# Kernel tuning notes

Measured on AMD Instinct MI355X. Metric: run time of the kernel, lower is better.

The kernel has to match this reference:

```python
import jax, jax.numpy as jnp
import numpy as np

N = 3000          # num_nodes
B = 1             # batch
T_IN = 12
T_OUT = 12
F_IN = 2
F_OUT = 2
HEADS = 8
HID = 32          # hidden_dim (GAT out channels, LSTM hidden)
E = 32000         # directed edges (before self-loops)
NEG_SLOPE = 0.2   # PyG GATConv leaky_relu slope


def setup_inputs() -> dict:
    key = jax.random.key(0)
    ks = jax.random.split(key, 20)
    s = 0.1
    inp = {
        "X": jax.random.normal(ks[0], (B, N, T_IN, F_IN), jnp.float32),
        "edge_index": jax.random.randint(ks[1], (2, E), 0, N, dtype=jnp.int64),
        # GATConv params (shared lin for src/dst, concat=False -> bias of size HID)
        "gat_w": jax.random.normal(ks[2], (HEADS * HID, F_IN), jnp.float32) * s,
        "att_src": jax.random.normal(ks[3], (HEADS, HID), jnp.float32) * s,
        "att_dst": jax.random.normal(ks[4], (HEADS, HID), jnp.float32) * s,
        "gat_b": jax.random.normal(ks[5], (HID,), jnp.float32) * s,
        # 2-layer LSTM, PyTorch gate order (i, f, g, o)
        "w_ih0": jax.random.normal(ks[6], (4 * HID, HID), jnp.float32) * s,
        "w_hh0": jax.random.normal(ks[7], (4 * HID, HID), jnp.float32) * s,
        "b_ih0": jax.random.normal(ks[8], (4 * HID,), jnp.float32) * s,
        "b_hh0": jax.random.normal(ks[9], (4 * HID,), jnp.float32) * s,
        "w_ih1": jax.random.normal(ks[10], (4 * HID, HID), jnp.float32) * s,
        "w_hh1": jax.random.normal(ks[11], (4 * HID, HID), jnp.float32) * s,
        "b_ih1": jax.random.normal(ks[12], (4 * HID,), jnp.float32) * s,
        "b_hh1": jax.random.normal(ks[13], (4 * HID,), jnp.float32) * s,
        # final head: HID -> F_OUT * T_OUT
        "fc_w": jax.random.normal(ks[14], (F_OUT * T_OUT, HID), jnp.float32) * s,
        "fc_b": jax.random.normal(ks[15], (F_OUT * T_OUT,), jnp.float32) * s,
    }
    return inp


def _lstm_layer(xs, w_ih, w_hh, b_ih, b_hh):
    # xs: (T, BN, D) -> hidden states (T, BN, H)
    Hd = w_hh.shape[1]
    def step(carry, x):
        h, c = carry
        g = x @ w_ih.T + h @ w_hh.T + b_ih + b_hh
        i, f, gg, o = jnp.split(g, 4, axis=-1)
        c = jax.nn.sigmoid(f) * c + jax.nn.sigmoid(i) * jnp.tanh(gg)
        h = jax.nn.sigmoid(o) * jnp.tanh(c)
        return (h, c), h
    z = jnp.zeros((xs.shape[1], Hd), xs.dtype)
    _, hs = jax.lax.scan(step, (z, z), xs)
    return hs


def reference(X, edge_index, gat_w, att_src, att_dst, gat_b,
              w_ih0, w_hh0, b_ih0, b_hh0, w_ih1, w_hh1, b_ih1, b_hh1,
              fc_w, fc_b):
    Bb, Nn, T, F = X.shape
    BN = Bb * Nn
    H, C = att_src.shape

    # (T, BN, F), all timesteps processed at once (GAT params shared across t)
    Xr = X.transpose(2, 0, 1, 3).reshape(T, BN, F)
    h = (Xr @ gat_w.T).reshape(T, BN, H, C)          # shared lin for src/dst
    a_s = (h * att_src).sum(-1)                      # (T, BN, H)
    a_d = (h * att_dst).sum(-1)

    # add self-loops (PyG GATConv default) over all BN nodes
    loops = jnp.arange(BN, dtype=edge_index.dtype)
    src = jnp.concatenate([edge_index[0], loops])
    dst = jnp.concatenate([edge_index[1], loops])

    # edge attention logits, edge axis leading for segment ops: (Etot, T, H)
    e = jax.nn.leaky_relu(a_s[:, src] + a_d[:, dst], NEG_SLOPE)
    e = jnp.moveaxis(e, 1, 0)

    # segment softmax over incoming edges per destination node
    m = jax.ops.segment_max(e, dst, num_segments=BN)
    ex = jnp.exp(e - m[dst])
    den = jax.ops.segment_sum(ex, dst, num_segments=BN)
    alpha = ex / den[dst]                            # (Etot, T, H)

    h_node = jnp.moveaxis(h, 0, 1)                   # (BN, T, H, C)
    msg = alpha[..., None] * h_node[src]             # (Etot, T, H, C)
    agg = jax.ops.segment_sum(msg, dst, num_segments=BN)  # (BN, T, H, C)
    gat_out = agg.mean(2) + gat_b                    # concat=False -> head mean; (BN, T, C)

    # 2-layer LSTM over time
    xs = gat_out.transpose(1, 0, 2)                  # (T, BN, C)
    hs = _lstm_layer(xs, w_ih0, w_hh0, b_ih0, b_hh0)
    hs = _lstm_layer(hs, w_ih1, w_hh1, b_ih1, b_hh1)
    h_last = hs[-1]                                  # (BN, HID)

    out = h_last @ fc_w.T + fc_b                     # (BN, F_OUT*T_OUT)
    return out.reshape(Bb, Nn, T_OUT, F)
```

## Files before the change

### kernel.cpp

```cpp
#include <hip/hip_runtime.h>
#include <math.h>

#define N_NODES 3000
#define T_STEPS 12
#define F_INP 2
#define HEADS 8
#define HID 32
#define E_EDGES 32000
#define E_TOT (E_EDGES + N_NODES)
#define NEG_SLOPE 0.2f
#define OUT_F 24
#define SLOTS 48
#define CHUNKS 6
#define NT (N_NODES * T_STEPS)
#define WROW 33

__device__ __forceinline__ float sigm(float x) {
    return 1.0f / (1.0f + __expf(-x));
}
__device__ __forceinline__ float tanh_f(float x) {
    return 1.0f - 2.0f / (__expf(2.0f * x) + 1.0f);
}
__device__ __forceinline__ float rdlane(float v, int l) {
    return __int_as_float(__builtin_amdgcn_readlane(__float_as_int(v), l));
}

__global__ __launch_bounds__(1024) void k_pre(const int* __restrict__ ei,
                                              const float* __restrict__ X,
                                              const float* __restrict__ gat_w,
                                              const float* __restrict__ att_src,
                                              const float* __restrict__ att_dst,
                                              float2* __restrict__ Xt,
                                              float* __restrict__ proj,
                                              int* __restrict__ cnt,
                                              int* __restrict__ eslot) {
    int tid = threadIdx.x, b = blockIdx.x;
    if (b < 35) {
        int i = b * 1024 + tid;
        if (i < E_TOT) {
            int s, d;
            if (i < E_EDGES) { s = ei[i]; d = ei[E_EDGES + i]; }
            else             { s = i - E_EDGES; d = s; }
            int slot = atomicAdd(&cnt[d], 1);
            if (slot < SLOTS) eslot[d * SLOTS + slot] = s;
        }
    } else if (b <= 70) {
        int i = (b - 35) * 1024 + tid;
        if (i < NT) {
            int n = i / T_STEPS, t = i - n * T_STEPS;
            float2 v = *(const float2*)&X[(size_t)i * 2];
            Xt[(size_t)t * N_NODES + n] = v;
        }
    } else {
        if (tid < 32) {
            int h = tid & 7, w = tid >> 3;
            const float* att = (w < 2) ? att_src : att_dst;
            int f = w & 1;
            float s = 0.0f;
            for (int c = 0; c < 32; c++)
                s += gat_w[((h * 32 + c) * 2) + f] * att[h * 32 + c];
            proj[w * 8 + h] = s;
        }
    }
}

__global__ __launch_bounds__(256) void k_gat(const float2* __restrict__ Xt,
                                             const int* __restrict__ cnt,
                                             const int* __restrict__ eslot,
                                             const float* __restrict__ proj,
                                             const float* __restrict__ gat_w,
                                             const float* __restrict__ gat_b,
                                             float* __restrict__ gat_out) {
    int pair = blockIdx.x * 4 + (threadIdx.x >> 6);
    int t = pair / N_NODES, n = pair - t * N_NODES;
    int lane = threadIdx.x & 63;
    int h = lane >> 3, slot = lane & 7;
    int rs = n * SLOTS;
    int deg = cnt[n];
    const float2* Xp = Xt + (size_t)t * N_NODES;
    float ps0 = proj[h], ps1 = proj[8 + h];
    float pd0 = proj[16 + h], pd1 = proj[24 + h];
    float2 xd = Xp[n];
    float ad = fmaf(xd.x, pd0, xd.y * pd1);

    float x0c[CHUNKS], x1c[CHUNKS], sc[CHUNKS];
    float m = -1e30f;
    #pragma unroll
    for (int c = 0; c < CHUNKS; c++) {
        if (8 * c < deg) {
            int e = slot + 8 * c;
            int idx = rs + (e < deg ? e : deg - 1);
            int src = eslot[idx];
            float2 xv = Xp[src];
            x0c[c] = xv.x; x1c[c] = xv.y;
            float s = fmaf(xv.x, ps0, fmaf(xv.y, ps1, ad));
            s = (s > 0.0f) ? s : NEG_SLOPE * s;
            sc[c] = (e < deg) ? s : -1e30f;
            m = fmaxf(m, sc[c]);
        } else { x0c[c] = 0.0f; x1c[c] = 0.0f; sc[c] = -1e30f; }
    }
    m = fmaxf(m, __shfl_xor(m, 1, 64));
    m = fmaxf(m, __shfl_xor(m, 2, 64));
    m = fmaxf(m, __shfl_xor(m, 4, 64));

    float den = 0.0f, S0 = 0.0f, S1 = 0.0f;
    #pragma unroll
    for (int c = 0; c < CHUNKS; c++) {
        if (8 * c < deg) {
            float a = __expf(sc[c] - m);
            den += a;
            S0 = fmaf(a, x0c[c], S0);
            S1 = fmaf(a, x1c[c], S1);
        }
    }
    #pragma unroll
    for (int mm = 1; mm <= 4; mm <<= 1) {
        den += __shfl_xor(den, mm, 64);
        S0  += __shfl_xor(S0,  mm, 64);
        S1  += __shfl_xor(S1,  mm, 64);
    }
    float inv = 0.125f / den;
    float v0 = S0 * inv, v1 = S1 * inv;

    float a0[HEADS], a1[HEADS];
    #pragma unroll
    for (int hh = 0; hh < HEADS; hh++) {
        a0[hh] = rdlane(v0, hh * 8);
        a1[hh] = rdlane(v1, hh * 8);
    }

    int cc = lane & 31;
    float acc = gat_b[cc];
    #pragma unroll
    for (int hh = 0; hh < HEADS; hh++) {
        float2 g = *(const float2*)&gat_w[(hh * 32 + cc) * 2];
        acc = fmaf(a0[hh], g.x, fmaf(a1[hh], g.y, acc));
    }
    if (lane < 32)
        gat_out[((size_t)n * T_STEPS + t) * HID + cc] = acc;
}

__global__ __launch_bounds__(256, 3)
void k_lstm(const float* __restrict__ gat_out,
            const float* __restrict__ w_ih0,
            const float* __restrict__ w_hh0,
            const float* __restrict__ b_ih0,
            const float* __restrict__ b_hh0,
            const float* __restrict__ w_ih1,
            const float* __restrict__ w_hh1,
            const float* __restrict__ b_ih1,
            const float* __restrict__ b_hh1,
            const float* __restrict__ fc_w,
            const float* __restrict__ fc_b,
            float* __restrict__ out) {
    __shared__ float wl[128 * WROW];
    int tid = threadIdx.x;
    int lane = tid & 63;
    int n = blockIdx.x * 4 + (tid >> 6);
    int j = lane & 31, half = lane >> 5;
    int rowA = half * 64 + j;
    int rowB = rowA + 32;

    auto stage = [&](const float* __restrict__ src, int nfloats) {
        for (int base = tid * 4; base < nfloats; base += 1024) {
            float4 v = *(const float4*)&src[base];
            float* d = &wl[(base >> 5) * WROW + (base & 31)];
            d[0] = v.x; d[1] = v.y; d[2] = v.z; d[3] = v.w;
        }
    };
    auto loadrows = [&](float* wA, float* wB) {
        #pragma unroll
        for (int k = 0; k < 32; k++) wA[k] = wl[rowA * WROW + k];
        #pragma unroll
        for (int k = 0; k < 32; k++) wB[k] = wl[rowB * WROW + k];
    };

    float wA[32], wB[32];

    stage(w_ih0, 4096);
    __syncthreads();
    loadrows(wA, wB);
    float bA = b_ih0[rowA] + b_hh0[rowA];
    float bB = b_ih0[rowB] + b_hh0[rowB];
    float xrow[T_STEPS];
    #pragma unroll
    for (int t = 0; t < T_STEPS; t++)
        xrow[t] = gat_out[((size_t)n * T_STEPS + t) * HID + j];
    float gxa[T_STEPS], gxb[T_STEPS];
    #pragma unroll
    for (int t = 0; t < T_STEPS; t++) {
        float a = bA, b = bB;
        #pragma unroll
        for (int k = 0; k < 32; k++) {
            float xk = rdlane(xrow[t], k);
            a = fmaf(xk, wA[k], a);
            b = fmaf(xk, wB[k], b);
        }
        gxa[t] = a; gxb[t] = b;
    }
    __syncthreads();

    stage(w_hh0, 4096);
    __syncthreads();
    loadrows(wA, wB);
    float h = 0.0f, c = 0.0f;
    float h0s[T_STEPS];
    #pragma unroll
    for (int t = 0; t < T_STEPS; t++) {
        float gA0 = gxa[t], gB0 = gxb[t], gA1 = 0.0f, gB1 = 0.0f;
        #pragma unroll
        for (int k = 0; k < 16; k++) {
            float h0 = rdlane(h, k), h1 = rdlane(h, k + 16);
            gA0 = fmaf(h0, wA[k], gA0);      gA1 = fmaf(h1, wA[k + 16], gA1);
            gB0 = fmaf(h0, wB[k], gB0);      gB1 = fmaf(h1, wB[k + 16], gB1);
        }
        float gA = gA0 + gA1, gB = gB0 + gB1;
        float oA = __shfl_xor(gA, 32, 64);
        float oB = __shfl_xor(gB, 32, 64);
        float gi = half ? oA : gA;
        float gf = half ? oB : gB;
        float gg = half ? gA : oA;
        float go = half ? gB : oB;
        c = sigm(gf) * c + sigm(gi) * tanh_f(gg);
        h = sigm(go) * tanh_f(c);
        h0s[t] = h;
    }
    __syncthreads();

    stage(w_ih1, 4096);
    __syncthreads();
    loadrows(wA, wB);
    float bA1 = b_ih1[rowA] + b_hh1[rowA];
    float bB1 = b_ih1[rowB] + b_hh1[rowB];
    #pragma unroll
    for (int t = 0; t < T_STEPS; t++) {
        float a = bA1, b = bB1;
        #pragma unroll
        for (int k = 0; k < 32; k++) {
            float xk = rdlane(h0s[t], k);
            a = fmaf(xk, wA[k], a);
            b = fmaf(xk, wB[k], b);
        }
        gxa[t] = a; gxb[t] = b;
    }
    __syncthreads();

    stage(w_hh1, 4096);
    __syncthreads();
    loadrows(wA, wB);
    h = 0.0f; c = 0.0f;
    #pragma unroll
    for (int t = 0; t < T_STEPS; t++) {
        float gA0 = gxa[t], gB0 = gxb[t], gA1 = 0.0f, gB1 = 0.0f;
        #pragma unroll
        for (int k = 0; k < 16; k++) {
            float h0 = rdlane(h, k), h1 = rdlane(h, k + 16);
            gA0 = fmaf(h0, wA[k], gA0);      gA1 = fmaf(h1, wA[k + 16], gA1);
            gB0 = fmaf(h0, wB[k], gB0);      gB1 = fmaf(h1, wB[k + 16], gB1);
        }
        float gA = gA0 + gA1, gB = gB0 + gB1;
        float oA = __shfl_xor(gA, 32, 64);
        float oB = __shfl_xor(gB, 32, 64);
        float gi = half ? oA : gA;
        float gf = half ? oB : gB;
        float gg = half ? gA : oA;
        float go = half ? gB : oB;
        c = sigm(gf) * c + sigm(gi) * tanh_f(gg);
        h = sigm(go) * tanh_f(c);
    }
    __syncthreads();

    stage(fc_w, OUT_F * HID);
    __syncthreads();
    int o = (lane < OUT_F) ? lane : (OUT_F - 1);
    float acc = fc_b[o];
    #pragma unroll
    for (int k = 0; k < 32; k++) {
        float hk = rdlane(h, k);
        acc = fmaf(hk, wl[o * WROW + k], acc);
    }
    if (lane < OUT_F) out[(size_t)n * OUT_F + lane] = acc;
}

extern "C" void kernel_launch(void* const* d_in, const int* in_sizes, int n_in,
                              void* d_out, int out_size, void* d_ws, size_t ws_size,
                              hipStream_t stream) {
    (void)in_sizes; (void)n_in; (void)out_size; (void)ws_size;
    const float* X       = (const float*)d_in[0];
    const int*   ei      = (const int*)d_in[1];
    const float* gat_w   = (const float*)d_in[2];
    const float* att_src = (const float*)d_in[3];
    const float* att_dst = (const float*)d_in[4];
    const float* gat_b   = (const float*)d_in[5];
    const float* w_ih0   = (const float*)d_in[6];
    const float* w_hh0   = (const float*)d_in[7];
    const float* b_ih0   = (const float*)d_in[8];
    const float* b_hh0   = (const float*)d_in[9];
    const float* w_ih1   = (const float*)d_in[10];
    const float* w_hh1   = (const float*)d_in[11];
    const float* b_ih1   = (const float*)d_in[12];
    const float* b_hh1   = (const float*)d_in[13];
    const float* fc_w    = (const float*)d_in[14];
    const float* fc_b    = (const float*)d_in[15];
    float* out = (float*)d_out;

    char* ws = (char*)d_ws;
    size_t off = 0;
    auto alloc_f = [&](size_t n) { float* p = (float*)(ws + off); off += n * sizeof(float); return p; };
    auto alloc_i = [&](size_t n) { int* p = (int*)(ws + off); off += n * sizeof(int); return p; };

    float*  gat_out = alloc_f((size_t)NT * HID);
    float2* Xt      = (float2*)alloc_f((size_t)NT * 2);
    float*  proj    = alloc_f(32);
    int* cnt   = alloc_i(N_NODES);
    int* eslot = alloc_i((size_t)N_NODES * SLOTS);

    hipMemsetAsync(cnt, 0, N_NODES * sizeof(int), stream);
    k_pre<<<72, 1024, 0, stream>>>(ei, X, gat_w, att_src, att_dst,
                                   Xt, proj, cnt, eslot);
    k_gat<<<NT / 4, 256, 0, stream>>>(Xt, cnt, eslot, proj,
                                      gat_w, gat_b, gat_out);
    k_lstm<<<N_NODES / 4, 256, 0, stream>>>(gat_out, w_ih0, w_hh0, b_ih0, b_hh0,
                                            w_ih1, w_hh1, b_ih1, b_hh1,
                                            fc_w, fc_b, out);
}
```

Measured before the change: 149.5 us.

## Fuse GAT attention aggregation into the LSTM kernel per node

Removes the separate GAT kernel and computes each node's attention softmax and head-mixed output for all 12 timesteps inside the LSTM kernel, keeping xrow in registers instead of writing and re-reading the gat_out buffer. Edge source indices are loaded once per node and reused across timesteps, and staging of the first weight matrix overlaps with the GAT computation. This saves a launch and the intermediate global traffic, but the fused kernel has only 750 blocks, so the GAT work now runs with much less parallelism. It also adds register pressure under the 3-blocks-per-SM launch bound, and an empty asm barrier pins the weight registers.

```diff
diff --git a/kernel.cpp b/kernel.cpp
--- a/kernel.cpp
+++ b/kernel.cpp
@@ -64,95 +64,24 @@
     }
 }
 
-__global__ __launch_bounds__(256) void k_gat(const float2* __restrict__ Xt,
-                                             const int* __restrict__ cnt,
-                                             const int* __restrict__ eslot,
-                                             const float* __restrict__ proj,
-                                             const float* __restrict__ gat_w,
-                                             const float* __restrict__ gat_b,
-                                             float* __restrict__ gat_out) {
-    int pair = blockIdx.x * 4 + (threadIdx.x >> 6);
-    int t = pair / N_NODES, n = pair - t * N_NODES;
-    int lane = threadIdx.x & 63;
-    int h = lane >> 3, slot = lane & 7;
-    int rs = n * SLOTS;
-    int deg = cnt[n];
-    const float2* Xp = Xt + (size_t)t * N_NODES;
-    float ps0 = proj[h], ps1 = proj[8 + h];
-    float pd0 = proj[16 + h], pd1 = proj[24 + h];
-    float2 xd = Xp[n];
-    float ad = fmaf(xd.x, pd0, xd.y * pd1);
-
-    float x0c[CHUNKS], x1c[CHUNKS], sc[CHUNKS];
-    float m = -1e30f;
-    #pragma unroll
-    for (int c = 0; c < CHUNKS; c++) {
-        if (8 * c < deg) {
-            int e = slot + 8 * c;
-            int idx = rs + (e < deg ? e : deg - 1);
-            int src = eslot[idx];
-            float2 xv = Xp[src];
-            x0c[c] = xv.x; x1c[c] = xv.y;
-            float s = fmaf(xv.x, ps0, fmaf(xv.y, ps1, ad));
-            s = (s > 0.0f) ? s : NEG_SLOPE * s;
-            sc[c] = (e < deg) ? s : -1e30f;
-            m = fmaxf(m, sc[c]);
-        } else { x0c[c] = 0.0f; x1c[c] = 0.0f; sc[c] = -1e30f; }
-    }
-    m = fmaxf(m, __shfl_xor(m, 1, 64));
-    m = fmaxf(m, __shfl_xor(m, 2, 64));
-    m = fmaxf(m, __shfl_xor(m, 4, 64));
-
-    float den = 0.0f, S0 = 0.0f, S1 = 0.0f;
-    #pragma unroll
-    for (int c = 0; c < CHUNKS; c++) {
-        if (8 * c < deg) {
-            float a = __expf(sc[c] - m);
-            den += a;
-            S0 = fmaf(a, x0c[c], S0);
-            S1 = fmaf(a, x1c[c], S1);
-        }
-    }
-    #pragma unroll
-    for (int mm = 1; mm <= 4; mm <<= 1) {
-        den += __shfl_xor(den, mm, 64);
-        S0  += __shfl_xor(S0,  mm, 64);
-        S1  += __shfl_xor(S1,  mm, 64);
-    }
-    float inv = 0.125f / den;
-    float v0 = S0 * inv, v1 = S1 * inv;
-
-    float a0[HEADS], a1[HEADS];
-    #pragma unroll
-    for (int hh = 0; hh < HEADS; hh++) {
-        a0[hh] = rdlane(v0, hh * 8);
-        a1[hh] = rdlane(v1, hh * 8);
-    }
-
-    int cc = lane & 31;
-    float acc = gat_b[cc];
-    #pragma unroll
-    for (int hh = 0; hh < HEADS; hh++) {
-        float2 g = *(const float2*)&gat_w[(hh * 32 + cc) * 2];
-        acc = fmaf(a0[hh], g.x, fmaf(a1[hh], g.y, acc));
-    }
-    if (lane < 32)
-        gat_out[((size_t)n * T_STEPS + t) * HID + cc] = acc;
-}
-
 __global__ __launch_bounds__(256, 3)
-void k_lstm(const float* __restrict__ gat_out,
-            const float* __restrict__ w_ih0,
-            const float* __restrict__ w_hh0,
-            const float* __restrict__ b_ih0,
-            const float* __restrict__ b_hh0,
-            const float* __restrict__ w_ih1,
-            const float* __restrict__ w_hh1,
-            const float* __restrict__ b_ih1,
-            const float* __restrict__ b_hh1,
-            const float* __restrict__ fc_w,
-            const float* __restrict__ fc_b,
-            float* __restrict__ out) {
+void k_fused(const float2* __restrict__ Xt,
+             const int* __restrict__ cnt,
+             const int* __restrict__ eslot,
+             const float* __restrict__ proj,
+             const float* __restrict__ gat_w,
+             const float* __restrict__ gat_b,
+             const float* __restrict__ w_ih0,
+             const float* __restrict__ w_hh0,
+             const float* __restrict__ b_ih0,
+             const float* __restrict__ b_hh0,
+             const float* __restrict__ w_ih1,
+             const float* __restrict__ w_hh1,
+             const float* __restrict__ b_ih1,
+             const float* __restrict__ b_hh1,
+             const float* __restrict__ fc_w,
+             const float* __restrict__ fc_b,
+             float* __restrict__ out) {
     __shared__ float wl[128 * WROW];
     int tid = threadIdx.x;
     int lane = tid & 63;
@@ -173,19 +102,90 @@
         for (int k = 0; k < 32; k++) wA[k] = wl[rowA * WROW + k];
         #pragma unroll
         for (int k = 0; k < 32; k++) wB[k] = wl[rowB * WROW + k];
+        #pragma unroll
+        for (int k = 0; k < 32; k++)
+            asm volatile("" : "+v"(wA[k]), "+v"(wB[k]));
     };
 
+    stage(w_ih0, 4096);
+
+    float xrow[T_STEPS];
+    {
+        int hh8 = lane >> 3, slot = lane & 7;
+        int deg = cnt[n];
+        deg = (deg < SLOTS) ? deg : SLOTS;
+        int srcs[CHUNKS];
+        #pragma unroll
+        for (int c = 0; c < CHUNKS; c++) {
+            int e = slot + 8 * c;
+            int idx = n * SLOTS + ((e < deg) ? e : deg - 1);
+            srcs[c] = (8 * c < deg) ? eslot[idx] : 0;
+        }
+        float ps0 = proj[hh8], ps1 = proj[8 + hh8];
+        float pd0 = proj[16 + hh8], pd1 = proj[24 + hh8];
+        float gb = gat_b[j];
+        float gw0[HEADS], gw1[HEADS];
+        #pragma unroll
+        for (int hh = 0; hh < HEADS; hh++) {
+            float2 g = *(const float2*)&gat_w[(hh * 32 + j) * 2];
+            gw0[hh] = g.x; gw1[hh] = g.y;
+        }
+        for (int t = 0; t < T_STEPS; t++) {
+            const float2* Xp = Xt + (size_t)t * N_NODES;
+            float2 xd = Xp[n];
+            float ad = fmaf(xd.x, pd0, xd.y * pd1);
+            float x0c[CHUNKS], x1c[CHUNKS], sc[CHUNKS];
+            float m = -1e30f;
+            #pragma unroll
+            for (int c = 0; c < CHUNKS; c++) {
+                if (8 * c < deg) {
+                    int e = slot + 8 * c;
+                    float2 xv = Xp[srcs[c]];
+                    x0c[c] = xv.x; x1c[c] = xv.y;
+                    float s = fmaf(xv.x, ps0, fmaf(xv.y, ps1, ad));
+                    s = (s > 0.0f) ? s : NEG_SLOPE * s;
+                    sc[c] = (e < deg) ? s : -1e30f;
+                    m = fmaxf(m, sc[c]);
+                } else { x0c[c] = 0.0f; x1c[c] = 0.0f; sc[c] = -1e30f; }
+            }
+            m = fmaxf(m, __shfl_xor(m, 1, 64));
+            m = fmaxf(m, __shfl_xor(m, 2, 64));
+            m = fmaxf(m, __shfl_xor(m, 4, 64));
+            float den = 0.0f, S0 = 0.0f, S1 = 0.0f;
+            #pragma unroll
+            for (int c = 0; c < CHUNKS; c++) {
+                if (8 * c < deg) {
+                    float a = __expf(sc[c] - m);
+                    den += a;
+                    S0 = fmaf(a, x0c[c], S0);
+                    S1 = fmaf(a, x1c[c], S1);
+                }
+            }
+            #pragma unroll
+            for (int mm = 1; mm <= 4; mm <<= 1) {
+                den += __shfl_xor(den, mm, 64);
+                S0  += __shfl_xor(S0,  mm, 64);
+                S1  += __shfl_xor(S1,  mm, 64);
+            }
+            float inv = 0.125f / den;
+            float v0 = S0 * inv, v1 = S1 * inv;
+            float acc = gb;
+            #pragma unroll
+            for (int hh = 0; hh < HEADS; hh++) {
+                float a0 = rdlane(v0, hh * 8);
+                float a1 = rdlane(v1, hh * 8);
+                acc = fmaf(a0, gw0[hh], fmaf(a1, gw1[hh], acc));
+            }
+            xrow[t] = acc;
+        }
+    }
+    __syncthreads();
+
     float wA[32], wB[32];
 
-    stage(w_ih0, 4096);
-    __syncthreads();
     loadrows(wA, wB);
     float bA = b_ih0[rowA] + b_hh0[rowA];
     float bB = b_ih0[rowB] + b_hh0[rowB];
-    float xrow[T_STEPS];
-    #pragma unroll
-    for (int t = 0; t < T_STEPS; t++)
-        xrow[t] = gat_out[((size_t)n * T_STEPS + t) * HID + j];
     float gxa[T_STEPS], gxb[T_STEPS];
     #pragma unroll
     for (int t = 0; t < T_STEPS; t++) {
@@ -309,18 +309,16 @@
     auto alloc_f = [&](size_t n) { float* p = (float*)(ws + off); off += n * sizeof(float); return p; };
     auto alloc_i = [&](size_t n) { int* p = (int*)(ws + off); off += n * sizeof(int); return p; };
 
-    float*  gat_out = alloc_f((size_t)NT * HID);
-    float2* Xt      = (float2*)alloc_f((size_t)NT * 2);
-    float*  proj    = alloc_f(32);
+    float2* Xt   = (float2*)alloc_f((size_t)NT * 2);
+    float*  proj = alloc_f(32);
     int* cnt   = alloc_i(N_NODES);
     int* eslot = alloc_i((size_t)N_NODES * SLOTS);
 
     hipMemsetAsync(cnt, 0, N_NODES * sizeof(int), stream);
     k_pre<<<72, 1024, 0, stream>>>(ei, X, gat_w, att_src, att_dst,
                                    Xt, proj, cnt, eslot);
-    k_gat<<<NT / 4, 256, 0, stream>>>(Xt, cnt, eslot, proj,
-                                      gat_w, gat_b, gat_out);
-    k_lstm<<<N_NODES / 4, 256, 0, stream>>>(gat_out, w_ih0, w_hh0, b_ih0, b_hh0,
-                                            w_ih1, w_hh1, b_ih1, b_hh1,
-                                            fc_w, fc_b, out);
-}
+    k_fused<<<N_NODES / 4, 256, 0, stream>>>(Xt, cnt, eslot, proj, gat_w, gat_b,
+                                             w_ih0, w_hh0, b_ih0, b_hh0,
+                                             w_ih1, w_hh1, b_ih1, b_hh1,
+                                             fc_w, fc_b, out);
+}
```

Result: no change. 146.7 us (-1.9%).
